# Kernel tuning notes

Hardware: AMD Instinct MI355X
Metric: run time of the kernel (lower is better)

Reference implementation:

```python
import jax, jax.numpy as jnp
import numpy as np

OUT_F, IN_F = 8192, 8192
RATIO = 0.05


def setup_inputs() -> dict:
    rng = np.random.default_rng(0)
    # Simulate the quantization performed in OrthoLinear.__init__ with numpy.
    w = (rng.standard_normal((OUT_F, IN_F)) * 0.02).astype(np.float32)
    w_abs = np.abs(w)
    k_idx = min(int(IN_F * 0.995), IN_F - 1)
    # torch.kthvalue(k) = k-th smallest (1-indexed) -> partition index k-1
    robust_max = np.partition(w_abs, k_idx - 1, axis=1)[:, k_idx - 1][:, None]
    robust_max = np.maximum(robust_max, 1e-6)
    scales = (robust_max / 7.0).astype(np.float32)
    w_int = np.clip(np.round(w / scales), -7, 7).astype(np.float32)
    resid = w - w_int * scales
    # top-k |residual| entries form the sparse CSR correction
    k = max(int(resid.size * RATIO), 1)
    metric = np.abs(resid).ravel()
    idx = np.argpartition(metric, -k)[-k:]
    idx.sort()
    rows = idx // IN_F
    cols = (idx % IN_F).astype(np.int32)
    vals = resid.ravel()[idx].astype(np.float16)
    ptr = np.zeros(OUT_F + 1, np.int32)
    ptr[1:] = np.cumsum(np.bincount(rows, minlength=OUT_F)).astype(np.int32)
    # pack two int4 (offset by +8) per byte: even cols -> low nibble, odd -> high
    offs = (w_int + 8.0).astype(np.uint8)
    packed = (offs[:, 0::2] | (offs[:, 1::2] << 4)).astype(np.int32)
    x = jax.random.normal(jax.random.key(0), (4, 8, IN_F), jnp.float32)
    return {
        "x": x,
        "base_packed": jnp.asarray(packed),
        "scales": jnp.asarray(scales.reshape(-1)),
        "ortho_vals": jnp.asarray(vals),
        "ortho_indices": jnp.asarray(cols),
        "ortho_ptr": jnp.asarray(ptr),
        "alpha": jnp.float32(1.0),
    }


def reference(x, base_packed, scales, ortho_vals, ortho_indices, ortho_ptr, alpha):
    lead = x.shape[:-1]
    in_f = x.shape[-1]
    out_f = base_packed.shape[0]
    xf = x.reshape(-1, in_f).astype(jnp.float32)  # [N, in]
    # dequantize packed int4 base weight: interleave low/high nibbles
    low = base_packed & 0xF
    high = (base_packed >> 4) & 0xF
    w_int = jnp.stack([low, high], axis=-1).reshape(out_f, in_f).astype(jnp.float32) - 8.0
    w_base = w_int * scales[:, None]  # [out, in]
    # CSR residual -> scatter into dense [out, in] (disjoint coords), then GEMM
    nnz = ortho_vals.shape[0]
    row_ids = jnp.searchsorted(ortho_ptr, jnp.arange(nnz, dtype=jnp.int32), side="right") - 1
    w_res = jnp.zeros((out_f, in_f), jnp.float32).at[row_ids, ortho_indices].add(
        ortho_vals.astype(jnp.float32)
    )
    out = xf @ w_base.T + alpha * (xf @ w_res.T)  # [N, out]
    return out.reshape(lead + (out_f,))
```

## Files before the change

### kernel.cpp

```cpp
#include <hip/hip_runtime.h>
#include <hip/hip_fp16.h>


#define IN_F 8192
#define OUT_F 8192
#define NROW 32
#define KSPLIT 8
#define KSEG (IN_F / KSPLIT)
#define CHUNKS (KSEG / 32)

typedef __attribute__((ext_vector_type(8))) short short8v;
typedef __attribute__((ext_vector_type(4))) float f32x4;

union Frag {
  int4 v;
  unsigned int u[4];
  short8v s;
};

__device__ __forceinline__ unsigned int cvt_pk_bf16(float lo, float hi) {
  unsigned int r;
  asm("v_cvt_pk_bf16_f32 %0, %1, %2" : "=v"(r) : "v"(lo), "v"(hi));
  return r;
}

__device__ __forceinline__ unsigned short f2bf(float f) {
  unsigned int u = __float_as_uint(f);
  u += 0x7FFFu + ((u >> 16) & 1u);
  return (unsigned short)(u >> 16);
}

__global__ __launch_bounds__(256) void prep_kernel(
    const float* __restrict__ x, unsigned short* __restrict__ x_hi,
    unsigned short* __restrict__ x_lo, unsigned short* __restrict__ xTb,
    float* __restrict__ out) {
  int t = blockIdx.x * 256 + threadIdx.x;
  if (t < NROW * IN_F) {
    out[t] = 0.0f;
    float v = x[t];
    unsigned short h = f2bf(v);
    float hf = __uint_as_float((unsigned int)h << 16);
    unsigned short l = f2bf(v - hf);
    x_hi[t] = h;
    x_lo[t] = l;
    int n = t >> 13;
    int k = t & (IN_F - 1);
    xTb[k * NROW + n] = h;
  }
}

__global__ __launch_bounds__(256) void fused_kernel(
    const int* __restrict__ packed, const float* __restrict__ scales,
    const float* __restrict__ vals, const int* __restrict__ cols,
    const int* __restrict__ rptr, const float* __restrict__ alphap,
    const unsigned short* __restrict__ x_hi,
    const unsigned short* __restrict__ x_lo,
    const unsigned short* __restrict__ xTb, float* __restrict__ out) {
  __shared__ float red[4][64 * 33];
  int tid = threadIdx.x;
  int lane = tid & 63;
  int w = tid >> 6;
  int og = blockIdx.x >> 3;
  int g = blockIdx.x & 7;
  int lo16 = lane & 15;
  int lhi = lane >> 4;

  int o = og * 64 + w * 16 + lo16;
  int kbeg = g * KSEG;
  const int4* wp = (const int4*)(packed + (size_t)o * (IN_F / 2) + (kbeg >> 1)) + lhi;
  const unsigned short* xh = x_hi + lo16 * IN_F + kbeg + 8 * lhi;
  const unsigned short* xl = x_lo + lo16 * IN_F + kbeg + 8 * lhi;

  f32x4 acc0 = {0.f, 0.f, 0.f, 0.f};
  f32x4 acc1 = {0.f, 0.f, 0.f, 0.f};

  for (int c = 0; c < CHUNKS; ++c) {
    int4 p = wp[c * 4];
    Frag b;
    b.u[0] = cvt_pk_bf16((float)(p.x & 15) - 8.0f, (float)(p.x >> 4) - 8.0f);
    b.u[1] = cvt_pk_bf16((float)(p.y & 15) - 8.0f, (float)(p.y >> 4) - 8.0f);
    b.u[2] = cvt_pk_bf16((float)(p.z & 15) - 8.0f, (float)(p.z >> 4) - 8.0f);
    b.u[3] = cvt_pk_bf16((float)(p.w & 15) - 8.0f, (float)(p.w >> 4) - 8.0f);
    Frag a0h, a0l, a1h, a1l;
    a0h.v = *(const int4*)(xh + c * 32);
    a0l.v = *(const int4*)(xl + c * 32);
    a1h.v = *(const int4*)(xh + 16 * IN_F + c * 32);
    a1l.v = *(const int4*)(xl + 16 * IN_F + c * 32);
    acc0 = __builtin_amdgcn_mfma_f32_16x16x32_bf16(a0h.s, b.s, acc0, 0, 0, 0);
    acc0 = __builtin_amdgcn_mfma_f32_16x16x32_bf16(a0l.s, b.s, acc0, 0, 0, 0);
    acc1 = __builtin_amdgcn_mfma_f32_16x16x32_bf16(a1h.s, b.s, acc1, 0, 0, 0);
    acc1 = __builtin_amdgcn_mfma_f32_16x16x32_bf16(a1l.s, b.s, acc1, 0, 0, 0);
  }
  float sc = scales[o];
#pragma unroll
  for (int r = 0; r < 4; ++r) {
    int m = lhi * 4 + r;
    atomicAdd(&out[(size_t)m * OUT_F + o], sc * acc0[r]);
    atomicAdd(&out[(size_t)(m + 16) * OUT_F + o], sc * acc1[r]);
  }

  float alpha = alphap[0];
  float* R = red[w];
#pragma unroll 1
  for (int rr = 0; rr < 2; ++rr) {
    int ro = og * 64 + g * 8 + w * 2 + rr;
    int js = rptr[ro], je = rptr[ro + 1];
    float acc[32];
#pragma unroll
    for (int i = 0; i < 32; ++i) acc[i] = 0.f;
    for (int j = js + lane; j < je; j += 64) {
      float v = vals[j];
      int col = cols[j];
      const int4* xp = (const int4*)(xTb + col * NROW);
      int4 q0 = xp[0], q1 = xp[1], q2 = xp[2], q3 = xp[3];
#define UNP(dw, base)                                                      \
  {                                                                        \
    unsigned int ud = (unsigned int)(dw);                                  \
    acc[base] = fmaf(v, __uint_as_float(ud << 16), acc[base]);             \
    acc[base + 1] = fmaf(v, __uint_as_float(ud & 0xFFFF0000u), acc[base + 1]); \
  }
      UNP(q0.x, 0) UNP(q0.y, 2) UNP(q0.z, 4) UNP(q0.w, 6)
      UNP(q1.x, 8) UNP(q1.y, 10) UNP(q1.z, 12) UNP(q1.w, 14)
      UNP(q2.x, 16) UNP(q2.y, 18) UNP(q2.z, 20) UNP(q2.w, 22)
      UNP(q3.x, 24) UNP(q3.y, 26) UNP(q3.z, 28) UNP(q3.w, 30)
#undef UNP
    }
#pragma unroll
    for (int i = 0; i < 32; ++i) R[lane * 33 + i] = acc[i];
    __syncthreads();
    int cidx = lane & 31;
    int h = lane >> 5;
    float sum = 0.f;
#pragma unroll
    for (int r = 0; r < 32; ++r) sum += R[(h * 32 + r) * 33 + cidx];
    sum += __shfl_xor(sum, 32, 64);
    if (lane < 32) atomicAdd(&out[(size_t)lane * OUT_F + ro], alpha * sum);
    __syncthreads();
  }
}

extern "C" void kernel_launch(void* const* d_in, const int* in_sizes, int n_in,
                              void* d_out, int out_size, void* d_ws, size_t ws_size,
                              hipStream_t stream) {
  const float* x = (const float*)d_in[0];
  const int* packed = (const int*)d_in[1];
  const float* scales = (const float*)d_in[2];
  const float* vals = (const float*)d_in[3];
  const int* cols = (const int*)d_in[4];
  const int* rptr = (const int*)d_in[5];
  const float* alphap = (const float*)d_in[6];
  float* out = (float*)d_out;

  unsigned short* x_hi = (unsigned short*)d_ws;
  unsigned short* x_lo = x_hi + NROW * IN_F;
  unsigned short* xTb = x_lo + NROW * IN_F;

  prep_kernel<<<(NROW * IN_F + 255) / 256, 256, 0, stream>>>(x, x_hi, x_lo, xTb, out);
  fused_kernel<<<(OUT_F / 64) * KSPLIT, 256, 0, stream>>>(
      packed, scales, vals, cols, rptr, alphap, x_hi, x_lo, xTb, out);
}
```

Baseline: 296.4 us.

## Pipeline GEMM loads, prefetch sparse entries, LDS-transpose prep, drop block barriers

Rewrites the prep kernel to transpose x through shared memory, emitting vectorized xTb writes and float4 zeroing of the output. Double-buffers the int4 weight and activation fragment loads in the MFMA loop so loads for the next chunk overlap compute. Prefetches the next CSR value and column in the sparse loop and removes block-wide barriers around the per-wave reduction buffer. Removing the barriers depends on intra-wave LDS ordering being preserved.

```diff
diff --git a/kernel.cpp b/kernel.cpp
--- a/kernel.cpp
+++ b/kernel.cpp
@@ -1,5 +1,4 @@
 #include <hip/hip_runtime.h>
-#include <hip/hip_fp16.h>
 
 
 #define IN_F 8192
@@ -34,19 +33,43 @@
     const float* __restrict__ x, unsigned short* __restrict__ x_hi,
     unsigned short* __restrict__ x_lo, unsigned short* __restrict__ xTb,
     float* __restrict__ out) {
-  int t = blockIdx.x * 256 + threadIdx.x;
-  if (t < NROW * IN_F) {
-    out[t] = 0.0f;
-    float v = x[t];
+  __shared__ unsigned short T[64 * 33];
+  int tid = threadIdx.x;
+  int k0 = blockIdx.x * 64;
+
+  {
+    float4 z = {0.f, 0.f, 0.f, 0.f};
+    float4* o4 = (float4*)out;
+    o4[blockIdx.x * 512 + tid] = z;
+    o4[blockIdx.x * 512 + 256 + tid] = z;
+  }
+
+  int kk = tid & 63;
+  int ng = tid >> 6;
+#pragma unroll
+  for (int p = 0; p < 8; ++p) {
+    int n = p * 4 + ng;
+    int idx = n * IN_F + k0 + kk;
+    float v = x[idx];
     unsigned short h = f2bf(v);
     float hf = __uint_as_float((unsigned int)h << 16);
     unsigned short l = f2bf(v - hf);
-    x_hi[t] = h;
-    x_lo[t] = l;
-    int n = t >> 13;
-    int k = t & (IN_F - 1);
-    xTb[k * NROW + n] = h;
-  }
+    x_hi[idx] = h;
+    x_lo[idx] = l;
+    T[kk * 33 + n] = h;
+  }
+  __syncthreads();
+  int kr = tid >> 2, q = tid & 3;
+  unsigned int s0 = T[kr * 33 + q * 8 + 0], s1 = T[kr * 33 + q * 8 + 1];
+  unsigned int s2 = T[kr * 33 + q * 8 + 2], s3 = T[kr * 33 + q * 8 + 3];
+  unsigned int s4 = T[kr * 33 + q * 8 + 4], s5 = T[kr * 33 + q * 8 + 5];
+  unsigned int s6 = T[kr * 33 + q * 8 + 6], s7 = T[kr * 33 + q * 8 + 7];
+  int4 wv;
+  wv.x = (int)(s0 | (s1 << 16));
+  wv.y = (int)(s2 | (s3 << 16));
+  wv.z = (int)(s4 | (s5 << 16));
+  wv.w = (int)(s6 | (s7 << 16));
+  ((int4*)xTb)[(size_t)(k0 + kr) * 4 + q] = wv;
 }
 
 __global__ __launch_bounds__(256) void fused_kernel(
@@ -74,23 +97,41 @@
   f32x4 acc0 = {0.f, 0.f, 0.f, 0.f};
   f32x4 acc1 = {0.f, 0.f, 0.f, 0.f};
 
-  for (int c = 0; c < CHUNKS; ++c) {
-    int4 p = wp[c * 4];
-    Frag b;
-    b.u[0] = cvt_pk_bf16((float)(p.x & 15) - 8.0f, (float)(p.x >> 4) - 8.0f);
-    b.u[1] = cvt_pk_bf16((float)(p.y & 15) - 8.0f, (float)(p.y >> 4) - 8.0f);
-    b.u[2] = cvt_pk_bf16((float)(p.z & 15) - 8.0f, (float)(p.z >> 4) - 8.0f);
-    b.u[3] = cvt_pk_bf16((float)(p.w & 15) - 8.0f, (float)(p.w >> 4) - 8.0f);
-    Frag a0h, a0l, a1h, a1l;
-    a0h.v = *(const int4*)(xh + c * 32);
-    a0l.v = *(const int4*)(xl + c * 32);
-    a1h.v = *(const int4*)(xh + 16 * IN_F + c * 32);
-    a1l.v = *(const int4*)(xl + 16 * IN_F + c * 32);
-    acc0 = __builtin_amdgcn_mfma_f32_16x16x32_bf16(a0h.s, b.s, acc0, 0, 0, 0);
-    acc0 = __builtin_amdgcn_mfma_f32_16x16x32_bf16(a0l.s, b.s, acc0, 0, 0, 0);
-    acc1 = __builtin_amdgcn_mfma_f32_16x16x32_bf16(a1h.s, b.s, acc1, 0, 0, 0);
-    acc1 = __builtin_amdgcn_mfma_f32_16x16x32_bf16(a1l.s, b.s, acc1, 0, 0, 0);
-  }
+  Frag wA, h0A, l0A, h1A, l1A;
+  Frag wB, h0B, l0B, h1B, l1B;
+
+#define LOADIN(W_, H0, L0, H1, L1, c)                  \
+  W_.v = wp[(c) * 4];                                  \
+  H0.v = *(const int4*)(xh + (c) * 32);                \
+  L0.v = *(const int4*)(xl + (c) * 32);                \
+  H1.v = *(const int4*)(xh + 16 * IN_F + (c) * 32);    \
+  L1.v = *(const int4*)(xl + 16 * IN_F + (c) * 32);
+
+#define COMPUTE(W_, H0, L0, H1, L1)                                               \
+  {                                                                               \
+    Frag b;                                                                       \
+    b.u[0] = cvt_pk_bf16((float)(W_.v.x & 15) - 8.0f, (float)(W_.v.x >> 4) - 8.0f); \
+    b.u[1] = cvt_pk_bf16((float)(W_.v.y & 15) - 8.0f, (float)(W_.v.y >> 4) - 8.0f); \
+    b.u[2] = cvt_pk_bf16((float)(W_.v.z & 15) - 8.0f, (float)(W_.v.z >> 4) - 8.0f); \
+    b.u[3] = cvt_pk_bf16((float)(W_.v.w & 15) - 8.0f, (float)(W_.v.w >> 4) - 8.0f); \
+    acc0 = __builtin_amdgcn_mfma_f32_16x16x32_bf16(H0.s, b.s, acc0, 0, 0, 0);     \
+    acc0 = __builtin_amdgcn_mfma_f32_16x16x32_bf16(L0.s, b.s, acc0, 0, 0, 0);     \
+    acc1 = __builtin_amdgcn_mfma_f32_16x16x32_bf16(H1.s, b.s, acc1, 0, 0, 0);     \
+    acc1 = __builtin_amdgcn_mfma_f32_16x16x32_bf16(L1.s, b.s, acc1, 0, 0, 0);     \
+  }
+
+  LOADIN(wA, h0A, l0A, h1A, l1A, 0)
+  for (int c = 0; c < CHUNKS; c += 2) {
+    LOADIN(wB, h0B, l0B, h1B, l1B, c + 1)
+    COMPUTE(wA, h0A, l0A, h1A, l1A)
+    if (c + 2 < CHUNKS) {
+      LOADIN(wA, h0A, l0A, h1A, l1A, c + 2)
+    }
+    COMPUTE(wB, h0B, l0B, h1B, l1B)
+  }
+#undef LOADIN
+#undef COMPUTE
+
   float sc = scales[o];
 #pragma unroll
   for (int r = 0; r < 4; ++r) {
@@ -108,34 +149,42 @@
     float acc[32];
 #pragma unroll
     for (int i = 0; i < 32; ++i) acc[i] = 0.f;
-    for (int j = js + lane; j < je; j += 64) {
-      float v = vals[j];
-      int col = cols[j];
-      const int4* xp = (const int4*)(xTb + col * NROW);
+
+    int j = js + lane;
+    float vc = 0.f;
+    int cc = 0;
+    if (j < je) { vc = vals[j]; cc = cols[j]; }
+    while (j < je) {
+      int jn = j + 64;
+      float vn = 0.f;
+      int cn = 0;
+      if (jn < je) { vn = vals[jn]; cn = cols[jn]; }
+      const int4* xp = (const int4*)(xTb + (size_t)cc * NROW);
       int4 q0 = xp[0], q1 = xp[1], q2 = xp[2], q3 = xp[3];
-#define UNP(dw, base)                                                      \
-  {                                                                        \
-    unsigned int ud = (unsigned int)(dw);                                  \
-    acc[base] = fmaf(v, __uint_as_float(ud << 16), acc[base]);             \
-    acc[base + 1] = fmaf(v, __uint_as_float(ud & 0xFFFF0000u), acc[base + 1]); \
+#define UNP(dw, base)                                                          \
+  {                                                                            \
+    unsigned int ud = (unsigned int)(dw);                                      \
+    acc[base] = fmaf(vc, __uint_as_float(ud << 16), acc[base]);                \
+    acc[base + 1] = fmaf(vc, __uint_as_float(ud & 0xFFFF0000u), acc[base + 1]); \
   }
       UNP(q0.x, 0) UNP(q0.y, 2) UNP(q0.z, 4) UNP(q0.w, 6)
       UNP(q1.x, 8) UNP(q1.y, 10) UNP(q1.z, 12) UNP(q1.w, 14)
       UNP(q2.x, 16) UNP(q2.y, 18) UNP(q2.z, 20) UNP(q2.w, 22)
       UNP(q3.x, 24) UNP(q3.y, 26) UNP(q3.z, 28) UNP(q3.w, 30)
 #undef UNP
+      j = jn;
+      vc = vn;
+      cc = cn;
     }
 #pragma unroll
     for (int i = 0; i < 32; ++i) R[lane * 33 + i] = acc[i];
-    __syncthreads();
     int cidx = lane & 31;
     int h = lane >> 5;
     float sum = 0.f;
 #pragma unroll
-    for (int r = 0; r < 32; ++r) sum += R[(h * 32 + r) * 33 + cidx];
+    for (int r2 = 0; r2 < 32; ++r2) sum += R[(h * 32 + r2) * 33 + cidx];
     sum += __shfl_xor(sum, 32, 64);
     if (lane < 32) atomicAdd(&out[(size_t)lane * OUT_F + ro], alpha * sum);
-    __syncthreads();
   }
 }
 
@@ -155,7 +204,7 @@
   unsigned short* x_lo = x_hi + NROW * IN_F;
   unsigned short* xTb = x_lo + NROW * IN_F;
 
-  prep_kernel<<<(NROW * IN_F + 255) / 256, 256, 0, stream>>>(x, x_hi, x_lo, xTb, out);
+  prep_kernel<<<IN_F / 64, 256, 0, stream>>>(x, x_hi, x_lo, xTb, out);
   fused_kernel<<<(OUT_F / 64) * KSPLIT, 256, 0, stream>>>(
       packed, scales, vals, cols, rptr, alphap, x_hi, x_lo, xTb, out);
 }
```

Result: no change. 300.6 us (+1.4%).
